# Performance work log

Hardware: AMD Instinct MI355X
Metric: run time of the kernel (lower is better)

## Reference

```python
import jax, jax.numpy as jnp
import numpy as np

B, S, D, H = 4, 2048, 1024, 16
DH = D // H


def setup_inputs() -> dict:
    key = jax.random.key(0)
    ks = jax.random.split(key, 11)
    s = 1.0 / np.sqrt(D)
    return {
        "q": jax.random.normal(ks[0], (B, S, D), jnp.float32),
        "k": jax.random.normal(ks[1], (B, S, D), jnp.float32),
        "v": jax.random.normal(ks[2], (B, S, D), jnp.float32),
        "Wq": jax.random.normal(ks[3], (D, D), jnp.float32) * s,
        "bq": jnp.zeros((D,), jnp.float32),
        "Wk": jax.random.normal(ks[4], (D, D), jnp.float32) * s,
        "bk": jnp.zeros((D,), jnp.float32),
        "Wv": jax.random.normal(ks[5], (D, D), jnp.float32) * s,
        "bv": jnp.zeros((D,), jnp.float32),
        "Wo": jax.random.normal(ks[6], (D, D), jnp.float32) * s,
        "bo": jnp.zeros((D,), jnp.float32),
    }


def _split_heads(x):
    # (B, S, D) -> (B, H, S, DH)
    b, s, _ = x.shape
    return x.reshape(b, s, H, DH).transpose(0, 2, 1, 3)


def reference(q, k, v, Wq, bq, Wk, bk, Wv, bv, Wo, bo):
    # torch Linear: x @ W.T + b
    qh = _split_heads(q @ Wq.T + bq)
    kh = _split_heads(k @ Wk.T + bk)
    vh = _split_heads(v @ Wv.T + bv)
    scale = 1.0 / jnp.sqrt(jnp.asarray(DH, qh.dtype))
    scores = jnp.einsum("bhqd,bhkd->bhqk", qh, kh) * scale  # (B,H,S,S)
    probs = jax.nn.softmax(scores, axis=-1)
    ctx = jnp.einsum("bhqk,bhkd->bhqd", probs, vh)  # (B,H,S,DH)
    x = ctx.transpose(0, 2, 1, 3).reshape(q.shape[0], -1, D)
    return x @ Wo.T + bo
```

## Files before the change

kernel.cpp:

```cpp
#include <hip/hip_runtime.h>

typedef __bf16 bf16x8 __attribute__((ext_vector_type(8)));
typedef __bf16 bf16x4 __attribute__((ext_vector_type(4)));
typedef _Float16 f16x4v __attribute__((ext_vector_type(4)));
typedef float f32x4 __attribute__((ext_vector_type(4)));
typedef float f32x16 __attribute__((ext_vector_type(16)));
typedef unsigned short u16;
typedef unsigned int u32;

constexpr int Bc = 4, Sc = 2048, Dc = 1024, Hc = 16, DHc = 64;
constexpr int Mrows = Bc * Sc;

__device__ __forceinline__ u16 f2bf(float f) {
  u32 u = __float_as_uint(f);
  u = (u + 0x7fffu + ((u >> 16) & 1u)) >> 16;
  return (u16)u;
}

#define LDSP(p) ((__attribute__((address_space(3))) void*)(p))
#define GLBP(p) ((const __attribute__((address_space(1))) void*)(p))

__global__ __launch_bounds__(256) void cvt3_kernel(const float* __restrict__ a,
                                                   const float* __restrict__ b,
                                                   const float* __restrict__ c,
                                                   ushort4* __restrict__ out, int n4) {
  const float4* in = (const float4*)(blockIdx.y == 0 ? a : blockIdx.y == 1 ? b : c);
  ushort4* o = out + (size_t)blockIdx.y * n4;
  int stride = gridDim.x * blockDim.x;
  for (int i = blockIdx.x * blockDim.x + threadIdx.x; i < n4; i += stride) {
    float4 v = in[i];
    ushort4 r;
    r.x = f2bf(v.x); r.y = f2bf(v.y); r.z = f2bf(v.z); r.w = f2bf(v.w);
    o[i] = r;
  }
}

__global__ __launch_bounds__(256) void cvt4_kernel(const float* __restrict__ a,
                                                   const float* __restrict__ b,
                                                   const float* __restrict__ c,
                                                   const float* __restrict__ d,
                                                   ushort4* __restrict__ out, int n4) {
  const float4* in = (const float4*)(blockIdx.y == 0 ? a : blockIdx.y == 1 ? b
                                     : blockIdx.y == 2 ? c : d);
  ushort4* o = out + (size_t)blockIdx.y * n4;
  int stride = gridDim.x * blockDim.x;
  for (int i = blockIdx.x * blockDim.x + threadIdx.x; i < n4; i += stride) {
    float4 v = in[i];
    ushort4 r;
    r.x = f2bf(v.x); r.y = f2bf(v.y); r.z = f2bf(v.z); r.w = f2bf(v.w);
    o[i] = r;
  }
}

enum GemmMode { MODE_Q = 0, MODE_K = 1, MODE_V = 2, MODE_OUT = 3 };

template <int MODE>
__global__ __launch_bounds__(512, 2) void gemm_bt(const u16* __restrict__ A, const u16* __restrict__ Bt,
                                                  const float* __restrict__ bias,
                                                  void* __restrict__ Cout) {
  constexpr int K = 1024, NT = K / 32;
  __shared__ u16 lds[5 * 12288];

  const int wg = (blockIdx.x & 7) * 32 + (blockIdx.x >> 3);
  const int tm = wg >> 3, tn = wg & 7;
  const int row0 = tm << 8, col0 = tn << 7;

  const int t_ = threadIdx.x, w = t_ >> 6, l = t_ & 63;
  const int wm = w >> 1, wn = w & 1;
  const int fr = l & 15, fo = (l >> 4) << 3;
  const int srow = l >> 2;
  const int scol = ((l & 3) ^ ((l >> 3) & 3)) << 3;

  f32x4 acc[4][4] = {};

  auto stage = [&](int tile) {
    const int kt = tile << 5;
    u16* buf = &lds[(tile % 5) * 12288];
#pragma unroll
    for (int R = 0; R < 2; ++R)
      __builtin_amdgcn_global_load_lds(
          GLBP(A + (size_t)(row0 + R * 128 + w * 16 + srow) * K + kt + scol),
          LDSP(buf + R * 4096 + w * 512), 16, 0, 0);
    __builtin_amdgcn_global_load_lds(
        GLBP(Bt + (size_t)(col0 + w * 16 + srow) * K + kt + scol),
        LDSP(buf + 8192 + w * 512), 16, 0, 0);
  };

  stage(0); stage(1); stage(2); stage(3);

#pragma unroll 1
  for (int t = 0; t < NT; ++t) {
    if (t + 4 < NT) {
      stage(t + 4);
      asm volatile("s_waitcnt vmcnt(12)" ::: "memory");
    } else {
      const int rem = NT - 1 - t;
      if (rem == 3)      asm volatile("s_waitcnt vmcnt(9)" ::: "memory");
      else if (rem == 2) asm volatile("s_waitcnt vmcnt(6)" ::: "memory");
      else if (rem == 1) asm volatile("s_waitcnt vmcnt(3)" ::: "memory");
      else               asm volatile("s_waitcnt vmcnt(0)" ::: "memory");
    }
    __builtin_amdgcn_s_barrier();

    const u16* buf = &lds[(t % 5) * 12288];
    bf16x8 af[4], bf[4];
#pragma unroll
    for (int mi = 0; mi < 4; ++mi) {
      const int r = wm * 64 + mi * 16 + fr;
      af[mi] = *(const bf16x8*)((const char*)buf + r * 64 + ((fo * 2) ^ (((r >> 1) & 3) << 4)));
    }
#pragma unroll
    for (int ni = 0; ni < 4; ++ni) {
      const int r = wn * 64 + ni * 16 + fr;
      bf[ni] = *(const bf16x8*)((const char*)(buf + 8192) + r * 64 +
                                ((fo * 2) ^ (((r >> 1) & 3) << 4)));
    }
    __builtin_amdgcn_s_setprio(1);
#pragma unroll
    for (int mi = 0; mi < 4; ++mi)
#pragma unroll
      for (int ni = 0; ni < 4; ++ni)
        acc[mi][ni] = __builtin_amdgcn_mfma_f32_16x16x32_bf16(af[mi], bf[ni], acc[mi][ni], 0, 0, 0);
    __builtin_amdgcn_s_setprio(0);
    __builtin_amdgcn_s_barrier();
    asm volatile("" ::: "memory");
  }

  const int rgrp = (l >> 4) << 2;
#pragma unroll
  for (int ni = 0; ni < 4; ++ni) {
    const int n = col0 + wn * 64 + ni * 16 + fr;
    const float bv = bias[n];
#pragma unroll
    for (int mi = 0; mi < 4; ++mi) {
      const int mbase = row0 + wm * 64 + mi * 16 + rgrp;
      if (MODE == MODE_OUT) {
        float* O = (float*)Cout;
#pragma unroll
        for (int i = 0; i < 4; ++i) O[(size_t)(mbase + i) * Dc + n] = acc[mi][ni][i] + bv;
      } else if (MODE == MODE_V) {
        const int b = mbase >> 11, s = mbase & (Sc - 1);
        const int h = n >> 6, dh = n & 63;
        u16* Vt = (u16*)Cout;
        f16x4v pk;
#pragma unroll
        for (int i = 0; i < 4; ++i) pk[i] = (_Float16)(acc[mi][ni][i] + bv);
        *(f16x4v*)&Vt[((size_t)((b * Hc + h) * DHc + dh)) * Sc + s] = pk;
      } else {
        u16* Oh = (u16*)Cout;
#pragma unroll
        for (int i = 0; i < 4; ++i) {
          const int m = mbase + i;
          const int b = m >> 11, s = m & (Sc - 1);
          const int h = n >> 6, dh = n & 63;
          float vv = acc[mi][ni][i] + bv;
          if (MODE == MODE_Q) vv *= 0.125f * 1.44269504089f;
          Oh[((size_t)((b * Hc + h) * Sc + s)) * DHc + dh] = f2bf(vv);
        }
      }
    }
  }
}

__global__ __launch_bounds__(256, 2) void attn2_kernel(const u16* __restrict__ Qh,
                                                       const u16* __restrict__ Kh,
                                                       const u16* __restrict__ Vt,
                                                       u16* __restrict__ ctx) {
  __shared__ u16 smem[8192];
  u16* K_lds = smem;
  u16* V_lds = smem + 4096;

  const int wid = (blockIdx.x & 7) * 128 + (blockIdx.x >> 3);
  const int qt = wid & 15, bh = wid >> 4;
  const int t = threadIdx.x, w = t >> 6, l = t & 63;
  const int q = l & 31, h = l >> 5;
  const int q0 = qt * 128 + w * 32;

  bf16x8 qf[4];
  {
    const u16* qp = Qh + ((size_t)bh * Sc + q0 + q) * DHc + h * 8;
#pragma unroll
    for (int kk = 0; kk < 4; ++kk) qf[kk] = *(const bf16x8*)(qp + kk * 16);
  }

  f32x16 oacc[2] = {};
  float m_run = -3.0e38f, l_run = 0.f;

  const int lrow = l >> 3, lg = l & 7;

  for (int kt = 0; kt < Sc; kt += 64) {
    __syncthreads();
#pragma unroll
    for (int c = 0; c < 2; ++c) {
      const int rb = w * 16 + c * 8;
      const int row = rb + lrow;
      const int sg = lg ^ (row & 7);
      __builtin_amdgcn_global_load_lds(GLBP(Kh + ((size_t)bh * Sc + kt + row) * DHc + sg * 8),
                                       LDSP(&K_lds[rb * 64]), 16, 0, 0);
      __builtin_amdgcn_global_load_lds(GLBP(Vt + ((size_t)bh * DHc + row) * Sc + kt + sg * 8),
                                       LDSP(&V_lds[rb * 64]), 16, 0, 0);
    }
    __syncthreads();

    f32x16 sacc[2];
#pragma unroll
    for (int kt32 = 0; kt32 < 2; ++kt32) {
      f32x16 s_ = {};
      const int krow = kt32 * 32 + q;
      __builtin_amdgcn_s_setprio(1);
#pragma unroll
      for (int kk = 0; kk < 4; ++kk) {
        bf16x8 kf = *(const bf16x8*)&K_lds[krow * 64 + ((2 * kk + h) ^ (krow & 7)) * 8];
        s_ = __builtin_amdgcn_mfma_f32_32x32x16_bf16(kf, qf[kk], s_, 0, 0, 0);
      }
      __builtin_amdgcn_s_setprio(0);
      sacc[kt32] = s_;
    }

    float mx = sacc[0][0];
#pragma unroll
    for (int r = 1; r < 16; ++r) mx = fmaxf(mx, sacc[0][r]);
#pragma unroll
    for (int r = 0; r < 16; ++r) mx = fmaxf(mx, sacc[1][r]);
    mx = fmaxf(mx, __shfl_xor(mx, 32));
    if (__any(mx - m_run > 8.f)) {
      const float mnew = fmaxf(m_run, mx);
      const float corr = __builtin_amdgcn_exp2f(m_run - mnew);
      m_run = mnew;
      l_run *= corr;
#pragma unroll
      for (int dt = 0; dt < 2; ++dt)
#pragma unroll
        for (int r = 0; r < 16; ++r) oacc[dt][r] *= corr;
    }
    float sum = 0.f;
    f16x4v pa[2][4];
#pragma unroll
    for (int kt32 = 0; kt32 < 2; ++kt32)
#pragma unroll
      for (int kc = 0; kc < 4; ++kc)
#pragma unroll
        for (int j = 0; j < 4; ++j) {
          float pv = __builtin_amdgcn_exp2f(sacc[kt32][kc * 4 + j] - m_run);
          sum += pv;
          pa[kt32][kc][j] = (_Float16)pv;
        }
    sum += __shfl_xor(sum, 32);
    l_run += sum;

    __builtin_amdgcn_s_setprio(1);
#pragma unroll
    for (int kt32 = 0; kt32 < 2; ++kt32)
#pragma unroll
      for (int kc = 0; kc < 4; ++kc)
#pragma unroll
        for (int dt = 0; dt < 2; ++dt) {
          const int vrow = dt * 32 + q;
          f16x4v vf = *(const f16x4v*)&V_lds[vrow * 64 + ((kt32 * 4 + kc) ^ (vrow & 7)) * 8 + 4 * h];
          oacc[dt] = __builtin_amdgcn_mfma_f32_32x32x8f16(vf, pa[kt32][kc], oacc[dt], 0, 0, 0);
        }
    __builtin_amdgcn_s_setprio(0);
  }

  __syncthreads();
  const float inv = 1.f / l_run;
  u16* E = smem + w * 2048;
#pragma unroll
  for (int dt = 0; dt < 2; ++dt)
#pragma unroll
    for (int rg = 0; rg < 4; ++rg) {
      bf16x4 pk;
#pragma unroll
      for (int j = 0; j < 4; ++j) pk[j] = (__bf16)(oacc[dt][rg * 4 + j] * inv);
      const int dh0 = dt * 32 + rg * 8 + 4 * h;
      int byte = q * 128 + dh0 * 2;
      byte ^= (q & 7) << 4;
      *(bf16x4*)((char*)E + byte) = pk;
    }
  __syncthreads();
  const int b = bh >> 4, head = bh & 15;
  const size_t crow = ((size_t)(b * Sc + q0 + q)) * Dc + head * 64 + h * 32;
#pragma unroll
  for (int i = 0; i < 4; ++i) {
    const int g = (4 * h + i) ^ (q & 7);
    uint4 tv = *(const uint4*)((char*)E + q * 128 + g * 16);
    *(uint4*)((u16*)ctx + crow + i * 8) = tv;
  }
}

extern "C" void kernel_launch(void* const* d_in, const int* in_sizes, int n_in,
                              void* d_out, int out_size, void* d_ws, size_t ws_size,
                              hipStream_t stream) {
  const float* q  = (const float*)d_in[0];
  const float* k  = (const float*)d_in[1];
  const float* v  = (const float*)d_in[2];
  const float* Wq = (const float*)d_in[3];
  const float* bq = (const float*)d_in[4];
  const float* Wk = (const float*)d_in[5];
  const float* bk = (const float*)d_in[6];
  const float* Wv = (const float*)d_in[7];
  const float* bv = (const float*)d_in[8];
  const float* Wo = (const float*)d_in[9];
  const float* bo = (const float*)d_in[10];
  float* out = (float*)d_out;

  const size_t MK = (size_t)Mrows * Dc;
  const size_t WK = (size_t)Dc * Dc;
  u16* qb  = (u16*)d_ws;
  u16* kb  = qb + MK;
  u16* vb  = kb + MK;
  u16* Wqb = vb + MK;
  u16* Wkb = Wqb + WK;
  u16* Wvb = Wkb + WK;
  u16* Wob = Wvb + WK;
  u16* Qh  = Wob + WK;
  u16* Kh  = Qh + MK;
  u16* VtB = Kh + MK;
  u16* ctx = VtB + MK;

  cvt3_kernel<<<dim3(2048, 3), 256, 0, stream>>>(q, k, v, (ushort4*)qb, (int)(MK / 4));
  cvt4_kernel<<<dim3(512, 4), 256, 0, stream>>>(Wq, Wk, Wv, Wo, (ushort4*)Wqb, (int)(WK / 4));

  gemm_bt<MODE_Q><<<256, 512, 0, stream>>>(qb, Wqb, bq, (void*)Qh);
  gemm_bt<MODE_K><<<256, 512, 0, stream>>>(kb, Wkb, bk, (void*)Kh);
  gemm_bt<MODE_V><<<256, 512, 0, stream>>>(vb, Wvb, bv, (void*)VtB);

  attn2_kernel<<<1024, 256, 0, stream>>>(Qh, Kh, VtB, ctx);

  gemm_bt<MODE_OUT><<<256, 512, 0, stream>>>(ctx, Wob, bo, (void*)out);
}
```

Baseline: 233.2 us.

## Rewrite projection GEMM with 32x32 MFMA, 64-wide K tiles, and batched QKV launch

Replaces the GEMM kernel with a version using 32x32x16 bf16 MFMA, 64-wide K tiles with triple buffering, and prefetch loads interleaved across the k-substeps. The three Q/K/V projections now run as one launch over a 3-deep grid instead of three launches. The attention softmax also gets a tree-shaped max reduction and packed fp16 conversion of probabilities. Together these aim to cut launch overhead, LDS traffic per MFMA, and serial dependency chains, at the cost of more barriers per tile and a changed epilogue register layout.

New measurement: 230.8 us. Within noise of the previous version (-1.0%).

```diff
diff --git a/kernel.cpp b/kernel.cpp
--- a/kernel.cpp
+++ b/kernel.cpp
@@ -10,6 +10,8 @@
 
 constexpr int Bc = 4, Sc = 2048, Dc = 1024, Hc = 16, DHc = 64;
 constexpr int Mrows = Bc * Sc;
+constexpr size_t MK = (size_t)Mrows * Dc;
+constexpr size_t WK = (size_t)Dc * Dc;
 
 __device__ __forceinline__ u16 f2bf(float f) {
   u32 u = __float_as_uint(f);
@@ -52,14 +54,20 @@
   }
 }
 
-enum GemmMode { MODE_Q = 0, MODE_K = 1, MODE_V = 2, MODE_OUT = 3 };
-
-template <int MODE>
-__global__ __launch_bounds__(512, 2) void gemm_bt(const u16* __restrict__ A, const u16* __restrict__ Bt,
-                                                  const float* __restrict__ bias,
-                                                  void* __restrict__ Cout) {
-  constexpr int K = 1024, NT = K / 32;
-  __shared__ u16 lds[5 * 12288];
+template <int FUSED3>
+__global__ __launch_bounds__(512, 2) void gemm8(const u16* __restrict__ A0,
+                                                const u16* __restrict__ Bt0,
+                                                const float* __restrict__ b0,
+                                                const float* __restrict__ b1,
+                                                const float* __restrict__ b2,
+                                                void* __restrict__ out0) {
+  constexpr int K = 1024, NT = 16;
+  __shared__ u16 lds[3 * 24576];
+
+  const int y = FUSED3 ? (int)blockIdx.y : 3;
+  const u16* A = A0 + (FUSED3 ? (size_t)blockIdx.y * MK : 0);
+  const u16* Bt = Bt0 + (FUSED3 ? (size_t)blockIdx.y * WK : 0);
+  const float* bias = FUSED3 ? (y == 0 ? b0 : y == 1 ? b1 : b2) : b0;
 
   const int wg = (blockIdx.x & 7) * 32 + (blockIdx.x >> 3);
   const int tm = wg >> 3, tn = wg & 7;
@@ -67,99 +75,112 @@
 
   const int t_ = threadIdx.x, w = t_ >> 6, l = t_ & 63;
   const int wm = w >> 1, wn = w & 1;
-  const int fr = l & 15, fo = (l >> 4) << 3;
-  const int srow = l >> 2;
-  const int scol = ((l & 3) ^ ((l >> 3) & 3)) << 3;
-
-  f32x4 acc[4][4] = {};
-
-  auto stage = [&](int tile) {
-    const int kt = tile << 5;
-    u16* buf = &lds[(tile % 5) * 12288];
-#pragma unroll
-    for (int R = 0; R < 2; ++R)
-      __builtin_amdgcn_global_load_lds(
-          GLBP(A + (size_t)(row0 + R * 128 + w * 16 + srow) * K + kt + scol),
-          LDSP(buf + R * 4096 + w * 512), 16, 0, 0);
+  const int col = l & 31, hh = l >> 5;
+
+  f32x16 acc[2][2] = {};
+
+  auto stA = [&](int tile, int i) {
+    u16* buf = &lds[(tile % 3) * 24576];
+    const int c = (w * 4 + i) * 64 + l;
+    const int r = c >> 3, gl = c & 7;
     __builtin_amdgcn_global_load_lds(
-        GLBP(Bt + (size_t)(col0 + w * 16 + srow) * K + kt + scol),
-        LDSP(buf + 8192 + w * 512), 16, 0, 0);
+        GLBP(A + (size_t)(row0 + r) * K + (tile << 6) + ((gl ^ (r & 7)) << 3)),
+        LDSP(buf + (w * 4 + i) * 512), 16, 0, 0);
   };
-
-  stage(0); stage(1); stage(2); stage(3);
+  auto stB = [&](int tile, int i) {
+    u16* buf = &lds[(tile % 3) * 24576] + 16384;
+    const int c = (w * 2 + i) * 64 + l;
+    const int r = c >> 3, gl = c & 7;
+    __builtin_amdgcn_global_load_lds(
+        GLBP(Bt + (size_t)(col0 + r) * K + (tile << 6) + ((gl ^ (r & 7)) << 3)),
+        LDSP(buf + (w * 2 + i) * 512), 16, 0, 0);
+  };
+
+#pragma unroll
+  for (int i = 0; i < 4; ++i) stA(0, i);
+#pragma unroll
+  for (int i = 0; i < 2; ++i) stB(0, i);
+#pragma unroll
+  for (int i = 0; i < 4; ++i) stA(1, i);
+#pragma unroll
+  for (int i = 0; i < 2; ++i) stB(1, i);
+  asm volatile("s_waitcnt vmcnt(6)" ::: "memory");
+  __builtin_amdgcn_s_barrier();
+
+  const int ar0 = wm * 64 + col, ar1 = ar0 + 32;
+  const int br0 = wn * 64 + col, br1 = br0 + 32;
 
 #pragma unroll 1
   for (int t = 0; t < NT; ++t) {
-    if (t + 4 < NT) {
-      stage(t + 4);
-      asm volatile("s_waitcnt vmcnt(12)" ::: "memory");
-    } else {
-      const int rem = NT - 1 - t;
-      if (rem == 3)      asm volatile("s_waitcnt vmcnt(9)" ::: "memory");
-      else if (rem == 2) asm volatile("s_waitcnt vmcnt(6)" ::: "memory");
-      else if (rem == 1) asm volatile("s_waitcnt vmcnt(3)" ::: "memory");
-      else               asm volatile("s_waitcnt vmcnt(0)" ::: "memory");
-    }
-    __builtin_amdgcn_s_barrier();
-
-    const u16* buf = &lds[(t % 5) * 12288];
-    bf16x8 af[4], bf[4];
-#pragma unroll
-    for (int mi = 0; mi < 4; ++mi) {
-      const int r = wm * 64 + mi * 16 + fr;
-      af[mi] = *(const bf16x8*)((const char*)buf + r * 64 + ((fo * 2) ^ (((r >> 1) & 3) << 4)));
-    }
-#pragma unroll
-    for (int ni = 0; ni < 4; ++ni) {
-      const int r = wn * 64 + ni * 16 + fr;
-      bf[ni] = *(const bf16x8*)((const char*)(buf + 8192) + r * 64 +
-                                ((fo * 2) ^ (((r >> 1) & 3) << 4)));
-    }
-    __builtin_amdgcn_s_setprio(1);
-#pragma unroll
-    for (int mi = 0; mi < 4; ++mi)
-#pragma unroll
-      for (int ni = 0; ni < 4; ++ni)
-        acc[mi][ni] = __builtin_amdgcn_mfma_f32_16x16x32_bf16(af[mi], bf[ni], acc[mi][ni], 0, 0, 0);
-    __builtin_amdgcn_s_setprio(0);
-    __builtin_amdgcn_s_barrier();
-    asm volatile("" ::: "memory");
-  }
-
-  const int rgrp = (l >> 4) << 2;
-#pragma unroll
-  for (int ni = 0; ni < 4; ++ni) {
-    const int n = col0 + wn * 64 + ni * 16 + fr;
-    const float bv = bias[n];
-#pragma unroll
-    for (int mi = 0; mi < 4; ++mi) {
-      const int mbase = row0 + wm * 64 + mi * 16 + rgrp;
-      if (MODE == MODE_OUT) {
-        float* O = (float*)Cout;
-#pragma unroll
-        for (int i = 0; i < 4; ++i) O[(size_t)(mbase + i) * Dc + n] = acc[mi][ni][i] + bv;
-      } else if (MODE == MODE_V) {
-        const int b = mbase >> 11, s = mbase & (Sc - 1);
+    const u16* abuf = &lds[(t % 3) * 24576];
+    const u16* bbuf = abuf + 16384;
+#pragma unroll
+    for (int ks = 0; ks < 4; ++ks) {
+      bf16x8 a0 = *(const bf16x8*)&abuf[ar0 * 64 + ((((ks << 1) + hh) ^ (ar0 & 7)) << 3)];
+      bf16x8 a1 = *(const bf16x8*)&abuf[ar1 * 64 + ((((ks << 1) + hh) ^ (ar1 & 7)) << 3)];
+      bf16x8 bq0 = *(const bf16x8*)&bbuf[br0 * 64 + ((((ks << 1) + hh) ^ (br0 & 7)) << 3)];
+      bf16x8 bq1 = *(const bf16x8*)&bbuf[br1 * 64 + ((((ks << 1) + hh) ^ (br1 & 7)) << 3)];
+      if (t + 2 < NT) {
+        if (ks == 0) { stA(t + 2, 0); stA(t + 2, 1); }
+        else if (ks == 1) { stA(t + 2, 2); stA(t + 2, 3); }
+        else if (ks == 2) { stB(t + 2, 0); stB(t + 2, 1); }
+      }
+      __builtin_amdgcn_sched_barrier(0);
+      __builtin_amdgcn_s_barrier();
+      __builtin_amdgcn_sched_barrier(0);
+      __builtin_amdgcn_s_setprio(1);
+      acc[0][0] = __builtin_amdgcn_mfma_f32_32x32x16_bf16(a0, bq0, acc[0][0], 0, 0, 0);
+      acc[0][1] = __builtin_amdgcn_mfma_f32_32x32x16_bf16(a0, bq1, acc[0][1], 0, 0, 0);
+      acc[1][0] = __builtin_amdgcn_mfma_f32_32x32x16_bf16(a1, bq0, acc[1][0], 0, 0, 0);
+      acc[1][1] = __builtin_amdgcn_mfma_f32_32x32x16_bf16(a1, bq1, acc[1][1], 0, 0, 0);
+      __builtin_amdgcn_s_setprio(0);
+      __builtin_amdgcn_sched_barrier(0);
+      if (ks == 3) {
+        if (t + 2 < NT)      asm volatile("s_waitcnt vmcnt(6)" ::: "memory");
+        else if (t + 1 < NT) asm volatile("s_waitcnt vmcnt(0)" ::: "memory");
+      }
+      __builtin_amdgcn_s_barrier();
+    }
+  }
+
+#pragma unroll
+  for (int mi = 0; mi < 2; ++mi)
+#pragma unroll
+    for (int ni = 0; ni < 2; ++ni) {
+      const int n = col0 + wn * 64 + ni * 32 + col;
+      const float bv = bias[n];
+      const int mbase = row0 + wm * 64 + mi * 32 + 4 * hh;
+      if (y == 3) {
+        float* O = (float*)out0;
+#pragma unroll
+        for (int r = 0; r < 16; ++r) {
+          const int m = mbase + (r & 3) + 8 * (r >> 2);
+          O[(size_t)m * Dc + n] = acc[mi][ni][r] + bv;
+        }
+      } else if (y == 2) {
+        u16* Vt = (u16*)out0 + 2 * MK;
         const int h = n >> 6, dh = n & 63;
-        u16* Vt = (u16*)Cout;
-        f16x4v pk;
-#pragma unroll
-        for (int i = 0; i < 4; ++i) pk[i] = (_Float16)(acc[mi][ni][i] + bv);
-        *(f16x4v*)&Vt[((size_t)((b * Hc + h) * DHc + dh)) * Sc + s] = pk;
+#pragma unroll
+        for (int qg = 0; qg < 4; ++qg) {
+          const int s0 = mbase + 8 * qg;
+          const int b = s0 >> 11, s = s0 & (Sc - 1);
+          f16x4v pk;
+#pragma unroll
+          for (int r4 = 0; r4 < 4; ++r4) pk[r4] = (_Float16)(acc[mi][ni][qg * 4 + r4] + bv);
+          *(f16x4v*)&Vt[((size_t)((b * Hc + h) * DHc + dh)) * Sc + s] = pk;
+        }
       } else {
-        u16* Oh = (u16*)Cout;
-#pragma unroll
-        for (int i = 0; i < 4; ++i) {
-          const int m = mbase + i;
+        u16* Oh = (u16*)out0 + (size_t)y * MK;
+        const float scl = (y == 0) ? 0.125f * 1.44269504089f : 1.f;
+        const int h = n >> 6, dh = n & 63;
+#pragma unroll
+        for (int r = 0; r < 16; ++r) {
+          const int m = mbase + (r & 3) + 8 * (r >> 2);
           const int b = m >> 11, s = m & (Sc - 1);
-          const int h = n >> 6, dh = n & 63;
-          float vv = acc[mi][ni][i] + bv;
-          if (MODE == MODE_Q) vv *= 0.125f * 1.44269504089f;
-          Oh[((size_t)((b * Hc + h) * Sc + s)) * DHc + dh] = f2bf(vv);
+          Oh[((size_t)((b * Hc + h) * Sc + s)) * DHc + dh] = f2bf((acc[mi][ni][r] + bv) * scl);
         }
       }
     }
-  }
 }
 
 __global__ __launch_bounds__(256, 2) void attn2_kernel(const u16* __restrict__ Qh,
@@ -217,11 +238,25 @@
       sacc[kt32] = s_;
     }
 
-    float mx = sacc[0][0];
-#pragma unroll
-    for (int r = 1; r < 16; ++r) mx = fmaxf(mx, sacc[0][r]);
-#pragma unroll
-    for (int r = 0; r < 16; ++r) mx = fmaxf(mx, sacc[1][r]);
+    float mx;
+    {
+      float t0 = fmaxf(fmaxf(sacc[0][0], sacc[0][1]), sacc[0][2]);
+      float t1 = fmaxf(fmaxf(sacc[0][3], sacc[0][4]), sacc[0][5]);
+      float t2 = fmaxf(fmaxf(sacc[0][6], sacc[0][7]), sacc[0][8]);
+      float t3 = fmaxf(fmaxf(sacc[0][9], sacc[0][10]), sacc[0][11]);
+      float t4 = fmaxf(fmaxf(sacc[0][12], sacc[0][13]), sacc[0][14]);
+      float t5 = fmaxf(fmaxf(sacc[0][15], sacc[1][0]), sacc[1][1]);
+      float t6 = fmaxf(fmaxf(sacc[1][2], sacc[1][3]), sacc[1][4]);
+      float t7 = fmaxf(fmaxf(sacc[1][5], sacc[1][6]), sacc[1][7]);
+      float t8 = fmaxf(fmaxf(sacc[1][8], sacc[1][9]), sacc[1][10]);
+      float t9 = fmaxf(fmaxf(sacc[1][11], sacc[1][12]), sacc[1][13]);
+      float ta = fmaxf(sacc[1][14], sacc[1][15]);
+      float u0 = fmaxf(fmaxf(t0, t1), t2);
+      float u1 = fmaxf(fmaxf(t3, t4), t5);
+      float u2 = fmaxf(fmaxf(t6, t7), t8);
+      float u3 = fmaxf(t9, ta);
+      mx = fmaxf(fmaxf(u0, u1), fmaxf(u2, u3));
+    }
     mx = fmaxf(mx, __shfl_xor(mx, 32));
     if (__any(mx - m_run > 8.f)) {
       const float mnew = fmaxf(m_run, mx);
@@ -238,13 +273,19 @@
 #pragma unroll
     for (int kt32 = 0; kt32 < 2; ++kt32)
 #pragma unroll
-      for (int kc = 0; kc < 4; ++kc)
-#pragma unroll
-        for (int j = 0; j < 4; ++j) {
-          float pv = __builtin_amdgcn_exp2f(sacc[kt32][kc * 4 + j] - m_run);
-          sum += pv;
-          pa[kt32][kc][j] = (_Float16)pv;
-        }
+      for (int kc = 0; kc < 4; ++kc) {
+        float p0 = __builtin_amdgcn_exp2f(sacc[kt32][kc * 4 + 0] - m_run);
+        float p1 = __builtin_amdgcn_exp2f(sacc[kt32][kc * 4 + 1] - m_run);
+        float p2 = __builtin_amdgcn_exp2f(sacc[kt32][kc * 4 + 2] - m_run);
+        float p3 = __builtin_amdgcn_exp2f(sacc[kt32][kc * 4 + 3] - m_run);
+        sum += (p0 + p1) + (p2 + p3);
+        auto lo = __builtin_amdgcn_cvt_pkrtz(p0, p1);
+        auto hi = __builtin_amdgcn_cvt_pkrtz(p2, p3);
+        f16x4v pk;
+        pk[0] = (_Float16)lo[0]; pk[1] = (_Float16)lo[1];
+        pk[2] = (_Float16)hi[0]; pk[3] = (_Float16)hi[1];
+        pa[kt32][kc] = pk;
+      }
     sum += __shfl_xor(sum, 32);
     l_run += sum;
 
@@ -304,16 +345,9 @@
   const float* bo = (const float*)d_in[10];
   float* out = (float*)d_out;
 
-  const size_t MK = (size_t)Mrows * Dc;
-  const size_t WK = (size_t)Dc * Dc;
   u16* qb  = (u16*)d_ws;
-  u16* kb  = qb + MK;
-  u16* vb  = kb + MK;
-  u16* Wqb = vb + MK;
-  u16* Wkb = Wqb + WK;
-  u16* Wvb = Wkb + WK;
-  u16* Wob = Wvb + WK;
-  u16* Qh  = Wob + WK;
+  u16* Wqb = qb + 3 * MK;
+  u16* Qh  = Wqb + 4 * WK;
   u16* Kh  = Qh + MK;
   u16* VtB = Kh + MK;
   u16* ctx = VtB + MK;
@@ -321,11 +355,9 @@
   cvt3_kernel<<<dim3(2048, 3), 256, 0, stream>>>(q, k, v, (ushort4*)qb, (int)(MK / 4));
   cvt4_kernel<<<dim3(512, 4), 256, 0, stream>>>(Wq, Wk, Wv, Wo, (ushort4*)Wqb, (int)(WK / 4));
 
-  gemm_bt<MODE_Q><<<256, 512, 0, stream>>>(qb, Wqb, bq, (void*)Qh);
-  gemm_bt<MODE_K><<<256, 512, 0, stream>>>(kb, Wkb, bk, (void*)Kh);
-  gemm_bt<MODE_V><<<256, 512, 0, stream>>>(vb, Wvb, bv, (void*)VtB);
+  gemm8<1><<<dim3(256, 3), 512, 0, stream>>>(qb, Wqb, bq, bk, bv, (void*)Qh);
 
   attn2_kernel<<<1024, 256, 0, stream>>>(Qh, Kh, VtB, ctx);
 
-  gemm_bt<MODE_OUT><<<256, 512, 0, stream>>>(ctx, Wob, bo, (void*)out);
-}
+  gemm8<0><<<dim3(256, 1), 512, 0, stream>>>(ctx, Wqb + 3 * WK, bo, bo, bo, (void*)out);
+}
```
